# Performance work log

Hardware: AMD Instinct MI355X
Metric: run time of the kernel (lower is better)

## Reference

```python
import jax, jax.numpy as jnp
import numpy as np
import math

BS, QLEN, DIM, NHEADS = 2, 2048, 1024, 16
DPH = DIM // NHEADS


def setup_inputs() -> dict:
    key = jax.random.key(0)
    ks = jax.random.split(key, 10)
    s = 0.02
    return {
        "input": jax.random.normal(ks[0], (BS, QLEN, DIM), jnp.float32),
        "mask": jax.random.randint(ks[1], (BS, QLEN), 0, 2, jnp.int32),
        "Wq": jax.random.normal(ks[2], (DIM, DIM), jnp.float32) * s,
        "bq": jnp.zeros((DIM,), jnp.float32),
        "Wk": jax.random.normal(ks[3], (DIM, DIM), jnp.float32) * s,
        "bk": jnp.zeros((DIM,), jnp.float32),
        "Wv": jax.random.normal(ks[4], (DIM, DIM), jnp.float32) * s,
        "bv": jnp.zeros((DIM,), jnp.float32),
        "Wo": jax.random.normal(ks[5], (DIM, DIM), jnp.float32) * s,
        "bo": jnp.zeros((DIM,), jnp.float32),
    }


def _shape(x):
    # (bs, len, dim) -> (bs, heads, len, dph)
    return x.reshape(BS, -1, NHEADS, DPH).transpose(0, 2, 1, 3)


def reference(input, mask, Wq, bq, Wk, bk, Wv, bv, Wo, bo):
    q = _shape(input @ Wq.T + bq)
    k = _shape(input @ Wk.T + bk)
    v = _shape(input @ Wv.T + bv)
    q = q / math.sqrt(DPH)
    scores = jnp.einsum("bhqd,bhkd->bhqk", q, k)  # (bs, h, qlen, klen)
    # original masked_fill_ with 1e-10 (NOT -inf)
    m = (mask == 0)[:, None, None, :]  # (bs,1,1,klen)
    scores = jnp.where(m, jnp.float32(1e-10), scores)
    weights = jax.nn.softmax(scores.astype(jnp.float32), axis=-1).astype(scores.dtype)
    # dropout p=0.0 / eval mode -> identity
    context = jnp.einsum("bhqk,bhkd->bhqd", weights, v)
    context = context.transpose(0, 2, 1, 3).reshape(BS, -1, DIM)
    return context @ Wo.T + bo
```

## Files before the change

kernel.cpp:

```cpp
#include <hip/hip_runtime.h>

typedef __attribute__((ext_vector_type(8))) _Float16 half8;
typedef __attribute__((ext_vector_type(4))) _Float16 half4;
typedef __attribute__((ext_vector_type(4))) float f32x4;
typedef __attribute__((ext_vector_type(16))) float f32x16;
typedef __attribute__((ext_vector_type(4))) int int4v;

#define BS 2
#define QLEN 2048
#define DIM 1024
#define NH 16
#define DPH 64
#define MTOT (BS * QLEN)
#define LOG2E 1.44269504088896340736f

__global__ void cvt_all(const float* __restrict__ x,
                        const float* __restrict__ wq, const float* __restrict__ wk,
                        const float* __restrict__ wv, const float* __restrict__ wo,
                        _Float16* __restrict__ X16,
                        _Float16* __restrict__ Wq16, _Float16* __restrict__ Wk16,
                        _Float16* __restrict__ Wv16, _Float16* __restrict__ Wo16) {
    const int NX = (MTOT * DIM) / 4;
    const int NW = (DIM * DIM) / 4;
    const int total = NX + 4 * NW;
    int idx = blockIdx.x * blockDim.x + threadIdx.x;
    int stride = gridDim.x * blockDim.x;
    for (int i = idx; i < total; i += stride) {
        const float* src; _Float16* dst; int off;
        if (i < NX) { src = x; dst = X16; off = i; }
        else {
            int k = i - NX; int which = k / NW; off = k - which * NW;
            src = which == 0 ? wq : which == 1 ? wk : which == 2 ? wv : wo;
            dst = which == 0 ? Wq16 : which == 1 ? Wk16 : which == 2 ? Wv16 : Wo16;
        }
        float4 v = ((const float4*)src)[off];
        half4 o;
        o[0] = (_Float16)v.x; o[1] = (_Float16)v.y;
        o[2] = (_Float16)v.z; o[3] = (_Float16)v.w;
        ((half4*)dst)[off] = o;
    }
}

__device__ __forceinline__ void gload_lds16(const _Float16* g, _Float16* l) {
    __builtin_amdgcn_global_load_lds(
        (const __attribute__((address_space(1))) void*)g,
        (__attribute__((address_space(3))) void*)l, 16, 0, 0);
}

__global__ __launch_bounds__(256) void gemm_qkv(
    const _Float16* __restrict__ A,
    const _Float16* __restrict__ Wq, const _Float16* __restrict__ Wk,
    const _Float16* __restrict__ Wv,
    const float* __restrict__ bq, const float* __restrict__ bk,
    const float* __restrict__ bv, const int* __restrict__ mask,
    _Float16* __restrict__ Qd, _Float16* __restrict__ Kd,
    _Float16* __restrict__ Vd) {
    const int K = 1024;
    __shared__ _Float16 sA[2][128 * 32];
    __shared__ _Float16 sB[2][128 * 32];
    const int z = blockIdx.z;
    const _Float16* W = (z == 0) ? Wq : (z == 1) ? Wk : Wv;
    const float* bias = (z == 0) ? bq : (z == 1) ? bk : bv;
    const int m0 = blockIdx.y * 128, n0 = blockIdx.x * 128;
    const int tid = threadIdx.x, w = tid >> 6, l = tid & 63;
    const int wr = (w >> 1) * 64, wc = (w & 1) * 64;
    const int r = l & 15, g = l >> 4;

    auto stage = [&](int k0, int bb) {
#pragma unroll
        for (int i = 0; i < 2; ++i) {
            int c = tid + i * 256;
            int row = c >> 2, seg = (c & 3) * 8;
            gload_lds16(&A[(size_t)(m0 + row) * K + k0 + seg], &sA[bb][c * 8]);
            gload_lds16(&W[(size_t)(n0 + row) * K + k0 + seg], &sB[bb][c * 8]);
        }
    };

    f32x4 acc[4][4] = {};

    stage(0, 0);
    __syncthreads();
    int buf = 0;
    for (int k0 = 0; k0 < K; k0 += 32) {
        if (k0 + 32 < K) stage(k0 + 32, buf ^ 1);

        half8 af[4], bf[4];
#pragma unroll
        for (int i = 0; i < 4; ++i) {
            af[i] = *(const half8*)&sA[buf][(wr + i * 16 + r) * 32 + g * 8];
            bf[i] = *(const half8*)&sB[buf][(wc + i * 16 + r) * 32 + g * 8];
        }
#pragma unroll
        for (int i = 0; i < 4; ++i)
#pragma unroll
            for (int j = 0; j < 4; ++j)
                acc[i][j] = __builtin_amdgcn_mfma_f32_16x16x32_f16(
                    af[i], bf[j], acc[i][j], 0, 0, 0);
        __syncthreads();
        buf ^= 1;
    }

    float bv4[4];
#pragma unroll
    for (int j = 0; j < 4; ++j) bv4[j] = bias[n0 + wc + j * 16 + r];

#pragma unroll
    for (int i = 0; i < 4; ++i)
#pragma unroll
        for (int j = 0; j < 4; ++j) {
            const int n = n0 + wc + j * 16 + r;
            const int h = n >> 6, d = n & 63;
#pragma unroll
            for (int reg = 0; reg < 4; ++reg) {
                const int m = m0 + wr + i * 16 + g * 4 + reg;
                const int bb = m >> 11, tt = m & 2047;
                float v = acc[i][j][reg] + bv4[j];
                if (z == 0)
                    Qd[(((size_t)(bb * NH + h)) * QLEN + tt) * DPH + d] =
                        (_Float16)(v * (0.125f * LOG2E));
                else if (z == 1) {
                    v = mask[bb * QLEN + tt] ? v : 0.f;
                    Kd[(((size_t)(bb * NH + h)) * QLEN + tt) * DPH + d] = (_Float16)v;
                } else
                    Vd[(((size_t)(bb * NH + h)) * DPH + d) * QLEN + tt] = (_Float16)v;
            }
        }
}

__global__ __launch_bounds__(256) void gemm_out(
    const _Float16* __restrict__ A, const _Float16* __restrict__ W,
    const float* __restrict__ bias, float* __restrict__ out) {
    const int K = 1024;
    __shared__ _Float16 sA[2][64 * 32];
    __shared__ _Float16 sB[2][128 * 32];
    const int m0 = blockIdx.y * 64, n0 = blockIdx.x * 128;
    const int tid = threadIdx.x, w = tid >> 6, l = tid & 63;
    const int wr = (w >> 1) * 32, wc = (w & 1) * 64;
    const int r = l & 15, g = l >> 4;

    auto stage = [&](int k0, int bb) {
        {
            int c = tid;
            int row = c >> 2, seg = (c & 3) * 8;
            gload_lds16(&A[(size_t)(m0 + row) * K + k0 + seg], &sA[bb][c * 8]);
        }
#pragma unroll
        for (int i = 0; i < 2; ++i) {
            int c = tid + i * 256;
            int row = c >> 2, seg = (c & 3) * 8;
            gload_lds16(&W[(size_t)(n0 + row) * K + k0 + seg], &sB[bb][c * 8]);
        }
    };

    f32x4 acc[2][4] = {};

    stage(0, 0);
    __syncthreads();
    int buf = 0;
    for (int k0 = 0; k0 < K; k0 += 32) {
        if (k0 + 32 < K) stage(k0 + 32, buf ^ 1);

        half8 af[2], bf[4];
#pragma unroll
        for (int i = 0; i < 2; ++i)
            af[i] = *(const half8*)&sA[buf][(wr + i * 16 + r) * 32 + g * 8];
#pragma unroll
        for (int j = 0; j < 4; ++j)
            bf[j] = *(const half8*)&sB[buf][(wc + j * 16 + r) * 32 + g * 8];
#pragma unroll
        for (int i = 0; i < 2; ++i)
#pragma unroll
            for (int j = 0; j < 4; ++j)
                acc[i][j] = __builtin_amdgcn_mfma_f32_16x16x32_f16(
                    af[i], bf[j], acc[i][j], 0, 0, 0);
        __syncthreads();
        buf ^= 1;
    }

    float bv4[4];
#pragma unroll
    for (int j = 0; j < 4; ++j) bv4[j] = bias[n0 + wc + j * 16 + r];
#pragma unroll
    for (int i = 0; i < 2; ++i)
#pragma unroll
        for (int j = 0; j < 4; ++j) {
            const int n = n0 + wc + j * 16 + r;
#pragma unroll
            for (int reg = 0; reg < 4; ++reg) {
                const int m = m0 + wr + i * 16 + g * 4 + reg;
                out[(size_t)m * DIM + n] = acc[i][j][reg] + bv4[j];
            }
        }
}

__global__ __launch_bounds__(512) void attn_kernel(
    const _Float16* __restrict__ Qg, const _Float16* __restrict__ Kg,
    const _Float16* __restrict__ Vg, _Float16* __restrict__ ctx) {
    __shared__ __align__(16) char smem[65536];

    const int flat = blockIdx.x;
    const int qt = (flat >> 3) & 15;
    const int bh = ((flat >> 7) << 3) | (flat & 7);
    const int b = bh >> 4, h = bh & 15;
    const _Float16* __restrict__ Qp = Qg + (size_t)bh * QLEN * DPH;
    const _Float16* __restrict__ Kp = Kg + (size_t)bh * QLEN * DPH;
    const _Float16* __restrict__ Vp = Vg + (size_t)bh * DPH * QLEN;

    const int tid = threadIdx.x, w = tid >> 6, l = tid & 63;
    const int qsub = w & 3, ksplit = w >> 2;
    const int ln = l & 31, hi = l >> 5;
    const int q0 = qt * 128 + qsub * 32;
    const int kbase = ksplit * 1024;

    _Float16* sK0 = (_Float16*)(smem + ksplit * 2 * 8192);
    _Float16* sV0 = (_Float16*)(smem + 32768 + ksplit * 2 * 8192);

    half8 qf[4];
#pragma unroll
    for (int ks = 0; ks < 4; ++ks)
        qf[ks] = *(const half8*)&Qp[(size_t)(q0 + ln) * DPH + ks * 16 + hi * 8];

    f32x16 accT[2] = {};
    float lsum = 0.f;

    const _Float16* kptr[2][4];
    const _Float16* vptr[2][2][2];
#pragma unroll
    for (int kb = 0; kb < 2; ++kb) {
#pragma unroll
        for (int ks = 0; ks < 4; ++ks)
            kptr[kb][ks] = sK0 + (kb * 32 + ln) * 64 + ((ks * 2 + hi) ^ (ln & 7)) * 8;
#pragma unroll
        for (int dblk = 0; dblk < 2; ++dblk) {
            vptr[kb][dblk][0] =
                sV0 + (dblk * 32 + ln) * 64 + ((kb * 4 + 0 + hi) ^ (ln & 7)) * 8;
            vptr[kb][dblk][1] =
                sV0 + (dblk * 32 + ln) * 64 + ((kb * 4 + 2 + hi) ^ (ln & 7)) * 8;
        }
    }

    const int c8 = ((l & 7) ^ (l >> 3)) * 8;
    const int rl = l >> 3;
    const _Float16* gK[2];
    const _Float16* gV[2];
    _Float16* dK[2];
    _Float16* dV[2];
#pragma unroll
    for (int j = 0; j < 2; ++j) {
        const int r0 = qsub * 16 + j * 8;
        gK[j] = &Kp[(size_t)(kbase + r0 + rl) * DPH + c8];
        gV[j] = &Vp[(size_t)(r0 + rl) * QLEN + kbase + c8];
        dK[j] = sK0 + r0 * 64 + l * 8;
        dV[j] = sV0 + r0 * 64 + l * 8;
    }

    auto stageAdv = [&](int bb) {
#pragma unroll
        for (int j = 0; j < 2; ++j) {
            gload_lds16(gK[j], dK[j] + bb * 4096);
            gload_lds16(gV[j], dV[j] + bb * 4096);
            gK[j] += 64 * DPH;
            gV[j] += 64;
        }
    };

    auto compute = [&](int bb) {
        const int boff = bb * 4096;
#pragma unroll
        for (int kb = 0; kb < 2; ++kb) {
            f32x16 st = {};
            __builtin_amdgcn_s_setprio(1);
#pragma unroll
            for (int ks = 0; ks < 4; ++ks) {
                half8 kf = *(const half8*)(kptr[kb][ks] + boff);
                st = __builtin_amdgcn_mfma_f32_32x32x16_f16(kf, qf[ks], st, 0, 0, 0);
            }
            __builtin_amdgcn_s_setprio(0);

            int cpk[8];
#pragma unroll
            for (int i = 0; i < 8; ++i) {
                float e0 = __builtin_amdgcn_exp2f(st[2 * i]);
                float e1 = __builtin_amdgcn_exp2f(st[2 * i + 1]);
                lsum += e0 + e1;
                cpk[i] =
                    __builtin_bit_cast(int, __builtin_amdgcn_cvt_pkrtz(e0, e1));
            }
            asm("v_permlane32_swap_b32 %0, %1" : "+v"(cpk[0]), "+v"(cpk[2]));
            asm("v_permlane32_swap_b32 %0, %1" : "+v"(cpk[1]), "+v"(cpk[3]));
            asm("v_permlane32_swap_b32 %0, %1" : "+v"(cpk[4]), "+v"(cpk[6]));
            asm("v_permlane32_swap_b32 %0, %1" : "+v"(cpk[5]), "+v"(cpk[7]));
            int4v b0 = {cpk[0], cpk[1], cpk[2], cpk[3]};
            int4v b1 = {cpk[4], cpk[5], cpk[6], cpk[7]};
            half8 Bf0 = __builtin_bit_cast(half8, b0);
            half8 Bf1 = __builtin_bit_cast(half8, b1);

            __builtin_amdgcn_s_setprio(1);
#pragma unroll
            for (int dblk = 0; dblk < 2; ++dblk) {
                half8 vf0 = *(const half8*)(vptr[kb][dblk][0] + boff);
                half8 vf1 = *(const half8*)(vptr[kb][dblk][1] + boff);
                accT[dblk] = __builtin_amdgcn_mfma_f32_32x32x16_f16(
                    vf0, Bf0, accT[dblk], 0, 0, 0);
                accT[dblk] = __builtin_amdgcn_mfma_f32_32x32x16_f16(
                    vf1, Bf1, accT[dblk], 0, 0, 0);
            }
            __builtin_amdgcn_s_setprio(0);
        }
    };

    stageAdv(0);
    __syncthreads();
    for (int t = 0; t < 8; ++t) {
        stageAdv(1);
        compute(0);
        __syncthreads();
        stageAdv(0);
        compute(1);
        __syncthreads();
    }

    lsum += __shfl_xor(lsum, 32);

    float* sRed = (float*)smem;
    if (ksplit == 1) {
        float* p = sRed + (qsub * 64 + l) * 33;
#pragma unroll
        for (int dblk = 0; dblk < 2; ++dblk)
#pragma unroll
            for (int i = 0; i < 16; ++i)
                p[dblk * 16 + i] = accT[dblk][i];
        p[32] = lsum;
    }
    __syncthreads();
    if (ksplit == 1) return;

    const float* p = sRed + (qsub * 64 + l) * 33;
#pragma unroll
    for (int dblk = 0; dblk < 2; ++dblk)
#pragma unroll
        for (int i = 0; i < 16; ++i)
            accT[dblk][i] += p[dblk * 16 + i];
    lsum += p[32];

    const float inv = 1.f / lsum;
    _Float16* cp = ctx + ((size_t)(b * QLEN) + q0 + ln) * DIM + h * DPH;
#pragma unroll
    for (int dblk = 0; dblk < 2; ++dblk)
#pragma unroll
        for (int j = 0; j < 4; ++j) {
            half4 o4;
#pragma unroll
            for (int e = 0; e < 4; ++e)
                o4[e] = (_Float16)(accT[dblk][4 * j + e] * inv);
            *(half4*)&cp[dblk * 32 + 8 * j + 4 * hi] = o4;
        }
}

extern "C" void kernel_launch(void* const* d_in, const int* in_sizes, int n_in,
                              void* d_out, int out_size, void* d_ws, size_t ws_size,
                              hipStream_t stream) {
    const float* x  = (const float*)d_in[0];
    const int* mask = (const int*)d_in[1];
    const float* Wq = (const float*)d_in[2];
    const float* bq = (const float*)d_in[3];
    const float* Wk = (const float*)d_in[4];
    const float* bk = (const float*)d_in[5];
    const float* Wv = (const float*)d_in[6];
    const float* bv = (const float*)d_in[7];
    const float* Wo = (const float*)d_in[8];
    const float* bo = (const float*)d_in[9];
    float* out = (float*)d_out;

    char* ws = (char*)d_ws;
    const size_t MB = 1u << 20;
    _Float16* X16  = (_Float16*)(ws + 0);
    _Float16* Wq16 = (_Float16*)(ws + 8 * MB);
    _Float16* Wk16 = (_Float16*)(ws + 10 * MB);
    _Float16* Wv16 = (_Float16*)(ws + 12 * MB);
    _Float16* Wo16 = (_Float16*)(ws + 14 * MB);
    _Float16* Q16  = (_Float16*)(ws + 16 * MB);
    _Float16* K16  = (_Float16*)(ws + 24 * MB);
    _Float16* V16T = (_Float16*)(ws + 32 * MB);
    _Float16* CTX  = (_Float16*)(ws + 40 * MB);

    cvt_all<<<2048, 256, 0, stream>>>(x, Wq, Wk, Wv, Wo,
                                      X16, Wq16, Wk16, Wv16, Wo16);

    gemm_qkv<<<dim3(8, 32, 3), 256, 0, stream>>>(
        X16, Wq16, Wk16, Wv16, bq, bk, bv, mask, Q16, K16, V16T);

    attn_kernel<<<512, 512, 0, stream>>>(Q16, K16, V16T, CTX);

    gemm_out<<<dim3(8, 64), 256, 0, stream>>>(CTX, Wo16, bo, out);
}
```

Measured before the change: 121.7 us.

## Swizzle LDS tiles, remap QKV GEMM blocks across XCDs, hoist load addressing

The QKV projection GEMM now XOR-swizzles the 8-half chunks in its LDS tiles so that fragment reads land in different banks. It also runs on a flat 768-block grid whose index is decoded so that blocks on the same XCD share A and W tiles for L2 reuse. Global and LDS addresses are precomputed once and advanced by pointer increments, and the K loop is unrolled by two with fixed buffer offsets. The final prefetch reads one tile past K, which is never used but touches adjacent workspace memory.

```diff
diff --git a/kernel.cpp b/kernel.cpp
--- a/kernel.cpp
+++ b/kernel.cpp
@@ -58,37 +58,64 @@
     const int K = 1024;
     __shared__ _Float16 sA[2][128 * 32];
     __shared__ _Float16 sB[2][128 * 32];
-    const int z = blockIdx.z;
+
+    const int flat = blockIdx.x;
+    const int xcd = flat & 7, seq = flat >> 3;
+    const int ya = xcd >> 1, nb = xcd & 1;
+    const int n_hi = seq & 3;
+    const int rem = seq >> 2;
+    const int z = rem % 3, y_hi = rem / 3;
+    const int y = y_hi * 4 + ya;
+    const int nblk = n_hi * 2 + nb;
+    const int m0 = y * 128, n0 = nblk * 128;
+
     const _Float16* W = (z == 0) ? Wq : (z == 1) ? Wk : Wv;
     const float* bias = (z == 0) ? bq : (z == 1) ? bk : bv;
-    const int m0 = blockIdx.y * 128, n0 = blockIdx.x * 128;
+
     const int tid = threadIdx.x, w = tid >> 6, l = tid & 63;
     const int wr = (w >> 1) * 64, wc = (w & 1) * 64;
     const int r = l & 15, g = l >> 4;
 
-    auto stage = [&](int k0, int bb) {
+    const _Float16* gA[2];
+    const _Float16* gW[2];
+    _Float16* dA[2];
+    _Float16* dB[2];
+#pragma unroll
+    for (int i = 0; i < 2; ++i) {
+        int s = tid + i * 256, row = s >> 2, pos = s & 3;
+        int chunk = pos ^ (row & 3);
+        gA[i] = &A[(size_t)(m0 + row) * K + chunk * 8];
+        gW[i] = &W[(size_t)(n0 + row) * K + chunk * 8];
+        dA[i] = &sA[0][s * 8];
+        dB[i] = &sB[0][s * 8];
+    }
+    auto stageAdv = [&](int bb) {
 #pragma unroll
         for (int i = 0; i < 2; ++i) {
-            int c = tid + i * 256;
-            int row = c >> 2, seg = (c & 3) * 8;
-            gload_lds16(&A[(size_t)(m0 + row) * K + k0 + seg], &sA[bb][c * 8]);
-            gload_lds16(&W[(size_t)(n0 + row) * K + k0 + seg], &sB[bb][c * 8]);
+            gload_lds16(gA[i], dA[i] + bb * 4096);
+            gload_lds16(gW[i], dB[i] + bb * 4096);
+            gA[i] += 32;
+            gW[i] += 32;
         }
     };
 
+    const int fpos = (g ^ (r & 3)) * 8;
+    const _Float16* pA[4];
+    const _Float16* pB[4];
+#pragma unroll
+    for (int i = 0; i < 4; ++i) {
+        pA[i] = &sA[0][(wr + i * 16 + r) * 32] + fpos;
+        pB[i] = &sB[0][(wc + i * 16 + r) * 32] + fpos;
+    }
+
     f32x4 acc[4][4] = {};
-
-    stage(0, 0);
-    __syncthreads();
-    int buf = 0;
-    for (int k0 = 0; k0 < K; k0 += 32) {
-        if (k0 + 32 < K) stage(k0 + 32, buf ^ 1);
-
+    auto compute = [&](int bb) {
+        const int boff = bb * 4096;
         half8 af[4], bf[4];
 #pragma unroll
         for (int i = 0; i < 4; ++i) {
-            af[i] = *(const half8*)&sA[buf][(wr + i * 16 + r) * 32 + g * 8];
-            bf[i] = *(const half8*)&sB[buf][(wc + i * 16 + r) * 32 + g * 8];
+            af[i] = *(const half8*)(pA[i] + boff);
+            bf[i] = *(const half8*)(pB[i] + boff);
         }
 #pragma unroll
         for (int i = 0; i < 4; ++i)
@@ -96,8 +123,17 @@
             for (int j = 0; j < 4; ++j)
                 acc[i][j] = __builtin_amdgcn_mfma_f32_16x16x32_f16(
                     af[i], bf[j], acc[i][j], 0, 0, 0);
+    };
+
+    stageAdv(0);
+    __syncthreads();
+    for (int t = 0; t < 16; ++t) {
+        stageAdv(1);
+        compute(0);
         __syncthreads();
-        buf ^= 1;
+        stageAdv(0);
+        compute(1);
+        __syncthreads();
     }
 
     float bv4[4];
@@ -387,7 +423,7 @@
     cvt_all<<<2048, 256, 0, stream>>>(x, Wq, Wk, Wv, Wo,
                                       X16, Wq16, Wk16, Wv16, Wo16);
 
-    gemm_qkv<<<dim3(8, 32, 3), 256, 0, stream>>>(
+    gemm_qkv<<<768, 256, 0, stream>>>(
         X16, Wq16, Wk16, Wv16, bq, bk, bv, mask, Q16, K16, V16T);
 
     attn_kernel<<<512, 512, 0, stream>>>(Q16, K16, V16T, CTX);
```

Result: no change. 122.1 us (+0.3%).
